# Performance work log

Measured on AMD Instinct MI355X. Metric: run time of the kernel, lower is better.

Reference implementation:

```python
import jax, jax.numpy as jnp
import numpy as np

N_NODES = 100000
N_EDGES = 1600000
IN_CH = 128
HID_CH = 128


def setup_inputs() -> dict:
    key = jax.random.key(0)
    ks = jax.random.split(key, 10)
    x = jax.random.normal(ks[0], (N_NODES, IN_CH), dtype=jnp.float32)
    edge_index = jax.random.randint(ks[1], (2, N_EDGES), 0, N_NODES, dtype=jnp.int64)
    s1 = 1.0 / np.sqrt(IN_CH)
    s2 = 1.0 / np.sqrt(HID_CH)
    return {
        "x": x,
        "edge_index": edge_index,
        "W1": jax.random.uniform(ks[2], (IN_CH, HID_CH), jnp.float32, -s1, s1),
        "b1": jnp.zeros((HID_CH,), jnp.float32),
        "W2": jax.random.uniform(ks[3], (HID_CH, HID_CH), jnp.float32, -s2, s2),
        "b2": jnp.zeros((HID_CH,), jnp.float32),
        "We": jax.random.uniform(ks[4], (IN_CH, HID_CH), jnp.float32, -s1, s1),
        "be": jax.random.uniform(ks[5], (HID_CH,), jnp.float32, -s1, s1),
        "Wfc": jax.random.uniform(ks[6], (HID_CH, 1), jnp.float32, -s2, s2),
        "bfc": jax.random.uniform(ks[7], (1,), jnp.float32, -s2, s2),
    }


def _gcn_conv(x, src, dst, norm, W, b, n_nodes):
    # PyG GCNConv: linear transform, then normalized scatter-add aggregation, then bias
    h = x @ W                                 # [N, H]
    msg = h[src] * norm[:, None]              # gather + scale  [E+N, H]
    out = jax.ops.segment_sum(msg, dst, num_segments=n_nodes)  # scatter-add [N, H]
    return out + b


def reference(x, edge_index, W1, b1, W2, b2, We, be, Wfc, bfc):
    n = x.shape[0]
    # add self-loops (PyG default add_self_loops=True)
    loop = jnp.arange(n, dtype=edge_index.dtype)
    src = jnp.concatenate([edge_index[0], loop])
    dst = jnp.concatenate([edge_index[1], loop])
    # symmetric degree normalization deg^-1/2 (edge_weight implicitly ones)
    deg = jax.ops.segment_sum(jnp.ones_like(src, dtype=x.dtype), dst, num_segments=n)
    dinv = jnp.where(deg > 0, jax.lax.rsqrt(deg), 0.0)
    norm = dinv[src] * dinv[dst]

    x_conv = jax.nn.relu(_gcn_conv(x, src, dst, norm, W1, b1, n))
    x_fc = jax.nn.relu(x @ We + be)
    h = x_conv + x_fc                          # residual; dropout is identity in eval
    x_conv2 = jax.nn.relu(_gcn_conv(h, src, dst, norm, W2, b2, n))
    h = x_conv2 + h
    # batch is all zeros -> global_mean_pool == mean over all nodes -> [1, H]
    pooled = jnp.mean(h, axis=0, keepdims=True)
    predict = jax.nn.sigmoid(pooled @ Wfc + bfc)  # [1, 1]
    return predict
```

## Files before the change

kernel.cpp:

```cpp
#include <hip/hip_runtime.h>
#include <hip/hip_bf16.h>

typedef unsigned int uint;
typedef unsigned short ushort;
typedef unsigned char uchar;
typedef __attribute__((ext_vector_type(8))) short short8;
typedef __attribute__((ext_vector_type(4))) float f32x4;

__device__ __forceinline__ float bf2f(ushort u) {
    union { uint i; float f; } v; v.i = ((uint)u) << 16; return v.f;
}
__device__ __forceinline__ ushort f2bf(float f) {
    union { float f; uint i; } v; v.f = f;
    uint x = v.i;
    uint r = (x + 0x7FFFu + ((x >> 16) & 1u)) >> 16;
    return (ushort)r;
}
__device__ __forceinline__ uchar f2q(float f) {
    return (uchar)(__builtin_amdgcn_cvt_pk_fp8_f32(f, 0.f, 0, false) & 0xFF);
}
__device__ __forceinline__ void q2f4(uint w, float* o) {
    o[0] = __builtin_amdgcn_cvt_f32_fp8(w, 0);
    o[1] = __builtin_amdgcn_cvt_f32_fp8(w, 1);
    o[2] = __builtin_amdgcn_cvt_f32_fp8(w, 2);
    o[3] = __builtin_amdgcn_cvt_f32_fp8(w, 3);
}


__global__ void k_degree(const int* __restrict__ dst, int* __restrict__ deg, int e) {
    int i = blockIdx.x * 256 + threadIdx.x;
    if (i < e) atomicAdd(&deg[dst[i]], 1);
}

__global__ void k_dinv(const int* __restrict__ deg, float* __restrict__ dinv, int n) {
    int i = blockIdx.x * 256 + threadIdx.x;
    if (i < n) dinv[i] = rsqrtf((float)deg[i] + 1.0f);
}

__global__ void k_scan_a(const int* __restrict__ deg, int* __restrict__ bsum, int n) {
    __shared__ int sd[256];
    int t = threadIdx.x;
    int base = blockIdx.x * 1024 + t * 4;
    int s = 0;
#pragma unroll
    for (int j = 0; j < 4; ++j) { int idx = base + j; if (idx < n) s += deg[idx]; }
    sd[t] = s; __syncthreads();
    for (int off = 1; off < 256; off <<= 1) {
        int v = (t >= off) ? sd[t - off] : 0;
        __syncthreads();
        sd[t] += v;
        __syncthreads();
    }
    if (t == 255) bsum[blockIdx.x] = sd[255];
}

__global__ void k_scan_b(const int* __restrict__ bsum, int* __restrict__ boff, int nb) {
    __shared__ int sd[256];
    int t = threadIdx.x;
    int v0 = (t < nb) ? bsum[t] : 0;
    sd[t] = v0; __syncthreads();
    for (int off = 1; off < 256; off <<= 1) {
        int v = (t >= off) ? sd[t - off] : 0;
        __syncthreads();
        sd[t] += v;
        __syncthreads();
    }
    if (t < nb) boff[t] = sd[t] - v0;
}

__global__ void k_scan_c(const int* __restrict__ deg, const int* __restrict__ boff,
                         int* __restrict__ offs, int n) {
    __shared__ int sd[256];
    int t = threadIdx.x;
    int base = blockIdx.x * 1024 + t * 4;
    int vals[4]; int s = 0;
#pragma unroll
    for (int j = 0; j < 4; ++j) {
        int idx = base + j;
        vals[j] = (idx < n) ? deg[idx] : 0;
        s += vals[j];
    }
    sd[t] = s; __syncthreads();
    for (int off = 1; off < 256; off <<= 1) {
        int v = (t >= off) ? sd[t - off] : 0;
        __syncthreads();
        sd[t] += v;
        __syncthreads();
    }
    int run = boff[blockIdx.x] + (sd[t] - s);
#pragma unroll
    for (int j = 0; j < 4; ++j) {
        int idx = base + j;
        if (idx < n) { offs[idx] = run; run += vals[j]; }
    }
}

__global__ void k_fill(const int* __restrict__ src, const int* __restrict__ dst,
                       const int* __restrict__ offs, int* __restrict__ cursor,
                       int* __restrict__ csr, int e) {
    int i = blockIdx.x * 256 + threadIdx.x;
    if (i < e) {
        int d = dst[i];
        int p = offs[d] + atomicAdd(&cursor[d], 1);
        csr[p] = src[i];
    }
}


__global__ __launch_bounds__(512) void k_gemm1(
    const float* __restrict__ x, const float* __restrict__ W1, const float* __restrict__ We,
    const float* __restrict__ be, const float* __restrict__ dinv,
    uchar* __restrict__ h1q, ushort* __restrict__ xfc, int n)
{
    __shared__ __align__(16) ushort Bt[256][72];
    int tid = threadIdx.x;
    int w = tid >> 6, lane = tid & 63;
    int ln15 = lane & 15, g = lane >> 4;
    int rowBase = blockIdx.x * 128 + w * 16;
    int r = rowBase + ln15;
    bool valid = r < n;

    short8 a[4];
#pragma unroll
    for (int ks = 0; ks < 4; ++ks) {
        float4 f0 = make_float4(0.f, 0.f, 0.f, 0.f), f1 = f0;
        if (valid) {
            const float* p = x + (size_t)r * 128 + ks * 32 + g * 8;
            f0 = *reinterpret_cast<const float4*>(p);
            f1 = *reinterpret_cast<const float4*>(p + 4);
        }
        short8 v;
        v[0] = (short)f2bf(f0.x); v[1] = (short)f2bf(f0.y);
        v[2] = (short)f2bf(f0.z); v[3] = (short)f2bf(f0.w);
        v[4] = (short)f2bf(f1.x); v[5] = (short)f2bf(f1.y);
        v[6] = (short)f2bf(f1.z); v[7] = (short)f2bf(f1.w);
        a[ks] = v;
    }

    f32x4 acc[16];
#pragma unroll
    for (int i = 0; i < 16; ++i) acc[i] = (f32x4){0.f, 0.f, 0.f, 0.f};

    for (int s = 0; s < 2; ++s) {
        for (int i = tid; i < 8192; i += 512) {
            int kl = i >> 7, j = i & 127;
            int kg = s * 64 + kl;
            Bt[j][kl]       = f2bf(W1[kg * 128 + j]);
            Bt[128 + j][kl] = f2bf(We[kg * 128 + j]);
        }
        __syncthreads();
#pragma unroll
        for (int t2 = 0; t2 < 2; ++t2) {
            short8 af = a[s * 2 + t2];
#pragma unroll
            for (int jf = 0; jf < 16; ++jf) {
                short8 bf = *reinterpret_cast<const short8*>(&Bt[jf * 16 + ln15][t2 * 32 + g * 8]);
                acc[jf] = __builtin_amdgcn_mfma_f32_16x16x32_bf16(af, bf, acc[jf], 0, 0, 0);
            }
        }
        __syncthreads();
    }

    float dv[4];
#pragma unroll
    for (int q = 0; q < 4; ++q) {
        int rr = rowBase + g * 4 + q;
        dv[q] = (rr < n) ? dinv[rr] : 0.f;
    }

#pragma unroll
    for (int jf = 0; jf < 16; ++jf) {
        int col = jf * 16 + ln15;
#pragma unroll
        for (int q = 0; q < 4; ++q) {
            int rr = rowBase + g * 4 + q;
            if (rr < n) {
                float v = acc[jf][q];
                if (col < 128) {
                    h1q[(size_t)rr * 128 + col] = f2q(v * dv[q]);
                } else {
                    float vv = fmaxf(v + be[col - 128], 0.f);
                    xfc[(size_t)rr * 128 + (col - 128)] = f2bf(vv);
                }
            }
        }
    }
}


__global__ __launch_bounds__(512) void k_gemm2(
    const ushort* __restrict__ h, const float* __restrict__ W2, const float* __restrict__ dinv,
    uchar* __restrict__ h2q, int n)
{
    __shared__ __align__(16) ushort Bt[128][72];
    int tid = threadIdx.x;
    int w = tid >> 6, lane = tid & 63;
    int ln15 = lane & 15, g = lane >> 4;
    int rowBase = blockIdx.x * 128 + w * 16;
    int r = rowBase + ln15;
    bool valid = r < n;

    short8 a[4];
#pragma unroll
    for (int ks = 0; ks < 4; ++ks) {
        short8 v = (short8){0,0,0,0,0,0,0,0};
        if (valid) v = *reinterpret_cast<const short8*>(h + (size_t)r * 128 + ks * 32 + g * 8);
        a[ks] = v;
    }

    f32x4 acc[8];
#pragma unroll
    for (int i = 0; i < 8; ++i) acc[i] = (f32x4){0.f, 0.f, 0.f, 0.f};

    for (int s = 0; s < 2; ++s) {
        for (int i = tid; i < 8192; i += 512) {
            int kl = i >> 7, j = i & 127;
            Bt[j][kl] = f2bf(W2[(s * 64 + kl) * 128 + j]);
        }
        __syncthreads();
#pragma unroll
        for (int t2 = 0; t2 < 2; ++t2) {
            short8 af = a[s * 2 + t2];
#pragma unroll
            for (int jf = 0; jf < 8; ++jf) {
                short8 bf = *reinterpret_cast<const short8*>(&Bt[jf * 16 + ln15][t2 * 32 + g * 8]);
                acc[jf] = __builtin_amdgcn_mfma_f32_16x16x32_bf16(af, bf, acc[jf], 0, 0, 0);
            }
        }
        __syncthreads();
    }

    float dv[4];
#pragma unroll
    for (int q = 0; q < 4; ++q) {
        int rr = rowBase + g * 4 + q;
        dv[q] = (rr < n) ? dinv[rr] : 0.f;
    }

#pragma unroll
    for (int jf = 0; jf < 8; ++jf) {
        int col = jf * 16 + ln15;
#pragma unroll
        for (int q = 0; q < 4; ++q) {
            int rr = rowBase + g * 4 + q;
            if (rr < n) h2q[(size_t)rr * 128 + col] = f2q(acc[jf][q] * dv[q]);
        }
    }
}


__global__ __launch_bounds__(256) void k_agg1(
    const int* __restrict__ csr, const int* __restrict__ offs, const int* __restrict__ degE,
    const float* __restrict__ dinv, const uchar* __restrict__ h1q, const ushort* __restrict__ xfc,
    const float* __restrict__ b1, ushort* __restrict__ h, int n)
{
    int t = threadIdx.x;
    int g = t >> 3, li = t & 7;
    int node = blockIdx.x * 32 + g;
    if (node >= n) return;
    int off = offs[node], cnt = degE[node];
    float di = dinv[node];
    int c0 = li * 16;
    float acc[16];
#pragma unroll
    for (int e = 0; e < 16; ++e) acc[e] = 0.f;

    for (int base = 0; base < cnt; base += 8) {
        int idx[8];
#pragma unroll
        for (int q = 0; q < 8; ++q) {
            int s = csr[off + base + q];
            idx[q] = (base + q < cnt) ? s : n;
        }
        uint4 u[8];
#pragma unroll
        for (int q = 0; q < 8; ++q)
            u[q] = *reinterpret_cast<const uint4*>(h1q + (size_t)idx[q] * 128 + c0);
#pragma unroll
        for (int q = 0; q < 8; ++q) {
            const uint* uw = reinterpret_cast<const uint*>(&u[q]);
#pragma unroll
            for (int p = 0; p < 4; ++p) {
                float d4[4]; q2f4(uw[p], d4);
                acc[4 * p + 0] += d4[0];
                acc[4 * p + 1] += d4[1];
                acc[4 * p + 2] += d4[2];
                acc[4 * p + 3] += d4[3];
            }
        }
    }

    uint4 us = *reinterpret_cast<const uint4*>(h1q + (size_t)node * 128 + c0);
    const uint* usw = reinterpret_cast<const uint*>(&us);
    float sdec[16];
#pragma unroll
    for (int p = 0; p < 4; ++p) q2f4(usw[p], &sdec[4 * p]);
    uint4 ux0 = *reinterpret_cast<const uint4*>(xfc + (size_t)node * 128 + c0);
    uint4 ux1 = *reinterpret_cast<const uint4*>(xfc + (size_t)node * 128 + c0 + 8);
    uint uxw[8] = {ux0.x, ux0.y, ux0.z, ux0.w, ux1.x, ux1.y, ux1.z, ux1.w};
    float bb[16];
#pragma unroll
    for (int p = 0; p < 4; ++p) {
        float4 bq = *reinterpret_cast<const float4*>(b1 + c0 + p * 4);
        bb[4 * p] = bq.x; bb[4 * p + 1] = bq.y; bb[4 * p + 2] = bq.z; bb[4 * p + 3] = bq.w;
    }
    uint outw[8];
#pragma unroll
    for (int j = 0; j < 8; ++j) {
        int e0 = 2 * j, e1 = 2 * j + 1;
        float v0 = fmaxf((acc[e0] + sdec[e0]) * di + bb[e0], 0.f) + bf2f((ushort)(uxw[j] & 0xffff));
        float v1 = fmaxf((acc[e1] + sdec[e1]) * di + bb[e1], 0.f) + bf2f((ushort)(uxw[j] >> 16));
        outw[j] = (uint)f2bf(v0) | ((uint)f2bf(v1) << 16);
    }
    ushort* hp = h + (size_t)node * 128 + c0;
    *reinterpret_cast<uint4*>(hp)     = make_uint4(outw[0], outw[1], outw[2], outw[3]);
    *reinterpret_cast<uint4*>(hp + 8) = make_uint4(outw[4], outw[5], outw[6], outw[7]);
}


__global__ __launch_bounds__(256) void k_agg2(
    const int* __restrict__ csr, const int* __restrict__ offs, const int* __restrict__ degE,
    const float* __restrict__ dinv, const uchar* __restrict__ h2q, const ushort* __restrict__ hres,
    const float* __restrict__ b2, float* __restrict__ pooled, int n)
{
    __shared__ float lpool[128];
    int t = threadIdx.x;
    if (t < 128) lpool[t] = 0.f;
    __syncthreads();
    int g = t >> 3, li = t & 7;
    int node = blockIdx.x * 32 + g;
    bool valid = node < n;
    int nodeC = valid ? node : (n - 1);
    int off = offs[nodeC];
    int cnt = valid ? degE[nodeC] : 0;
    float di = dinv[nodeC];
    int c0 = li * 16;
    float acc[16];
#pragma unroll
    for (int e = 0; e < 16; ++e) acc[e] = 0.f;

    for (int base = 0; base < cnt; base += 8) {
        int idx[8];
#pragma unroll
        for (int q = 0; q < 8; ++q) {
            int s = csr[off + base + q];
            idx[q] = (base + q < cnt) ? s : n;
        }
        uint4 u[8];
#pragma unroll
        for (int q = 0; q < 8; ++q)
            u[q] = *reinterpret_cast<const uint4*>(h2q + (size_t)idx[q] * 128 + c0);
#pragma unroll
        for (int q = 0; q < 8; ++q) {
            const uint* uw = reinterpret_cast<const uint*>(&u[q]);
#pragma unroll
            for (int p = 0; p < 4; ++p) {
                float d4[4]; q2f4(uw[p], d4);
                acc[4 * p + 0] += d4[0];
                acc[4 * p + 1] += d4[1];
                acc[4 * p + 2] += d4[2];
                acc[4 * p + 3] += d4[3];
            }
        }
    }

    uint4 us = *reinterpret_cast<const uint4*>(h2q + (size_t)nodeC * 128 + c0);
    const uint* usw = reinterpret_cast<const uint*>(&us);
    float sdec[16];
#pragma unroll
    for (int p = 0; p < 4; ++p) q2f4(usw[p], &sdec[4 * p]);
    uint4 ur0 = *reinterpret_cast<const uint4*>(hres + (size_t)nodeC * 128 + c0);
    uint4 ur1 = *reinterpret_cast<const uint4*>(hres + (size_t)nodeC * 128 + c0 + 8);
    uint urw[8] = {ur0.x, ur0.y, ur0.z, ur0.w, ur1.x, ur1.y, ur1.z, ur1.w};
    float bb[16];
#pragma unroll
    for (int p = 0; p < 4; ++p) {
        float4 bq = *reinterpret_cast<const float4*>(b2 + c0 + p * 4);
        bb[4 * p] = bq.x; bb[4 * p + 1] = bq.y; bb[4 * p + 2] = bq.z; bb[4 * p + 3] = bq.w;
    }
    float pv[16];
#pragma unroll
    for (int j = 0; j < 8; ++j) {
        int e0 = 2 * j, e1 = 2 * j + 1;
        pv[e0] = fmaxf((acc[e0] + sdec[e0]) * di + bb[e0], 0.f) + bf2f((ushort)(urw[j] & 0xffff));
        pv[e1] = fmaxf((acc[e1] + sdec[e1]) * di + bb[e1], 0.f) + bf2f((ushort)(urw[j] >> 16));
    }
    if (valid) {
#pragma unroll
        for (int e = 0; e < 16; ++e) atomicAdd(&lpool[c0 + e], pv[e]);
    }
    __syncthreads();
    if (t < 128) atomicAdd(&pooled[t], lpool[t]);
}


__global__ void k_final(const float* __restrict__ pooled, const float* __restrict__ Wfc,
                        const float* __restrict__ bfc, float* __restrict__ out, float invN) {
    int lane = threadIdx.x;
    float s = pooled[2 * lane] * invN * Wfc[2 * lane] +
              pooled[2 * lane + 1] * invN * Wfc[2 * lane + 1];
#pragma unroll
    for (int off = 32; off > 0; off >>= 1) s += __shfl_down(s, off);
    if (lane == 0) out[0] = 1.f / (1.f + expf(-(s + bfc[0])));
}


extern "C" void kernel_launch(void* const* d_in, const int* in_sizes, int n_in,
                              void* d_out, int out_size, void* d_ws, size_t ws_size,
                              hipStream_t stream) {
    const float* x   = (const float*)d_in[0];
    const int*   ei  = (const int*)d_in[1];
    const float* W1  = (const float*)d_in[2];
    const float* b1  = (const float*)d_in[3];
    const float* W2  = (const float*)d_in[4];
    const float* b2  = (const float*)d_in[5];
    const float* We  = (const float*)d_in[6];
    const float* be  = (const float*)d_in[7];
    const float* Wfc = (const float*)d_in[8];
    const float* bfc = (const float*)d_in[9];
    float* out = (float*)d_out;

    const int N = in_sizes[0] / 128;
    const int E = in_sizes[1] / 2;
    const int* src = ei;
    const int* dst = ei + E;

    char* w = (char*)d_ws;
    size_t off = 0;
    auto take = [&](size_t bytes) -> void* {
        void* p = w + off;
        off = (off + bytes + 255) & ~(size_t)255;
        return p;
    };
    int*    deg    = (int*)take((size_t)N * 4);
    int*    offs   = (int*)take((size_t)N * 4);
    int*    cursor = (int*)take((size_t)N * 4);
    float*  dinv   = (float*)take((size_t)N * 4);
    int*    bsum   = (int*)take(1024);
    int*    boff   = (int*)take(1024);
    int*    csr    = (int*)take((size_t)(E + 8) * 4);
    uchar*  h1q    = (uchar*)take((size_t)(N + 1) * 128);
    ushort* xfc    = (ushort*)take((size_t)N * 128 * 2);
    ushort* h      = (ushort*)take((size_t)N * 128 * 2);
    uchar*  h2q    = (uchar*)take((size_t)(N + 1) * 128);
    float*  pooled = (float*)take(512);

    const int nbE = (E + 255) / 256;
    const int nbScan = (N + 1023) / 1024;

    hipMemsetAsync(deg, 0, (size_t)N * 4, stream);
    hipMemsetAsync(cursor, 0, (size_t)N * 4, stream);
    hipMemsetAsync(pooled, 0, 512, stream);
    hipMemsetAsync(h1q + (size_t)N * 128, 0, 128, stream);
    hipMemsetAsync(h2q + (size_t)N * 128, 0, 128, stream);

    k_degree<<<nbE, 256, 0, stream>>>(dst, deg, E);
    k_dinv<<<(N + 255) / 256, 256, 0, stream>>>(deg, dinv, N);
    k_scan_a<<<nbScan, 256, 0, stream>>>(deg, bsum, N);
    k_scan_b<<<1, 256, 0, stream>>>(bsum, boff, nbScan);
    k_scan_c<<<nbScan, 256, 0, stream>>>(deg, boff, offs, N);
    k_fill<<<nbE, 256, 0, stream>>>(src, dst, offs, cursor, csr, E);

    k_gemm1<<<(N + 127) / 128, 512, 0, stream>>>(x, W1, We, be, dinv, h1q, xfc, N);
    k_agg1<<<(N + 31) / 32, 256, 0, stream>>>(csr, offs, deg, dinv, h1q, xfc, b1, h, N);
    k_gemm2<<<(N + 127) / 128, 512, 0, stream>>>(h, W2, dinv, h2q, N);
    k_agg2<<<(N + 31) / 32, 256, 0, stream>>>(csr, offs, deg, dinv, h2q, h, b2, pooled, N);
    k_final<<<1, 64, 0, stream>>>(pooled, Wfc, bfc, out, 1.0f / (float)N);
}
```

Measured before the change: 441.9 us.

## Bin degree/fill atomics by destination range and prefetch CSR indices in aggregation

```diff
diff --git a/kernel.cpp b/kernel.cpp
--- a/kernel.cpp
+++ b/kernel.cpp
@@ -27,9 +27,17 @@
 }
 
 
-__global__ void k_degree(const int* __restrict__ dst, int* __restrict__ deg, int e) {
-    int i = blockIdx.x * 256 + threadIdx.x;
-    if (i < e) atomicAdd(&deg[dst[i]], 1);
+__global__ void k_degree(const int* __restrict__ dst, int* __restrict__ deg,
+                         int e, int n) {
+    int bin = blockIdx.x & 7;
+    int sub = blockIdx.x >> 3;
+    int nsub = gridDim.x >> 3;
+    int q = (n + 7) >> 3;
+    int lo = bin * q, hi = min(n, lo + q);
+    for (int i = sub * 256 + threadIdx.x; i < e; i += nsub * 256) {
+        int d = dst[i];
+        if (d >= lo && d < hi) atomicAdd(&deg[d], 1);
+    }
 }
 
 __global__ void k_dinv(const int* __restrict__ deg, float* __restrict__ dinv, int n) {
@@ -97,12 +105,18 @@
 
 __global__ void k_fill(const int* __restrict__ src, const int* __restrict__ dst,
                        const int* __restrict__ offs, int* __restrict__ cursor,
-                       int* __restrict__ csr, int e) {
-    int i = blockIdx.x * 256 + threadIdx.x;
-    if (i < e) {
+                       int* __restrict__ csr, int e, int n) {
+    int bin = blockIdx.x & 7;
+    int sub = blockIdx.x >> 3;
+    int nsub = gridDim.x >> 3;
+    int q = (n + 7) >> 3;
+    int lo = bin * q, hi = min(n, lo + q);
+    for (int i = sub * 256 + threadIdx.x; i < e; i += nsub * 256) {
         int d = dst[i];
-        int p = offs[d] + atomicAdd(&cursor[d], 1);
-        csr[p] = src[i];
+        if (d >= lo && d < hi) {
+            int p = offs[d] + atomicAdd(&cursor[d], 1);
+            csr[p] = src[i];
+        }
     }
 }
 
@@ -265,17 +279,25 @@
 #pragma unroll
     for (int e = 0; e < 16; ++e) acc[e] = 0.f;
 
-    for (int base = 0; base < cnt; base += 8) {
-        int idx[8];
-#pragma unroll
-        for (int q = 0; q < 8; ++q) {
-            int s = csr[off + base + q];
-            idx[q] = (base + q < cnt) ? s : n;
-        }
+    int nbat = (cnt + 7) >> 3;
+    int idx[8];
+#pragma unroll
+    for (int q = 0; q < 8; ++q) {
+        int s = csr[off + q];
+        idx[q] = (q < cnt) ? s : n;
+    }
+    for (int b = 0; b < nbat; ++b) {
         uint4 u[8];
 #pragma unroll
         for (int q = 0; q < 8; ++q)
             u[q] = *reinterpret_cast<const uint4*>(h1q + (size_t)idx[q] * 128 + c0);
+        int base2 = (b + 1) * 8;
+        int idxn[8];
+#pragma unroll
+        for (int q = 0; q < 8; ++q) {
+            int s = csr[off + base2 + q];
+            idxn[q] = (base2 + q < cnt) ? s : n;
+        }
 #pragma unroll
         for (int q = 0; q < 8; ++q) {
             const uint* uw = reinterpret_cast<const uint*>(&u[q]);
@@ -288,6 +310,8 @@
                 acc[4 * p + 3] += d4[3];
             }
         }
+#pragma unroll
+        for (int q = 0; q < 8; ++q) idx[q] = idxn[q];
     }
 
     uint4 us = *reinterpret_cast<const uint4*>(h1q + (size_t)node * 128 + c0);
@@ -339,17 +363,25 @@
 #pragma unroll
     for (int e = 0; e < 16; ++e) acc[e] = 0.f;
 
-    for (int base = 0; base < cnt; base += 8) {
-        int idx[8];
-#pragma unroll
-        for (int q = 0; q < 8; ++q) {
-            int s = csr[off + base + q];
-            idx[q] = (base + q < cnt) ? s : n;
-        }
+    int nbat = (cnt + 7) >> 3;
+    int idx[8];
+#pragma unroll
+    for (int q = 0; q < 8; ++q) {
+        int s = csr[off + q];
+        idx[q] = (q < cnt) ? s : n;
+    }
+    for (int b = 0; b < nbat; ++b) {
         uint4 u[8];
 #pragma unroll
         for (int q = 0; q < 8; ++q)
             u[q] = *reinterpret_cast<const uint4*>(h2q + (size_t)idx[q] * 128 + c0);
+        int base2 = (b + 1) * 8;
+        int idxn[8];
+#pragma unroll
+        for (int q = 0; q < 8; ++q) {
+            int s = csr[off + base2 + q];
+            idxn[q] = (base2 + q < cnt) ? s : n;
+        }
 #pragma unroll
         for (int q = 0; q < 8; ++q) {
             const uint* uw = reinterpret_cast<const uint*>(&u[q]);
@@ -362,6 +394,8 @@
                 acc[4 * p + 3] += d4[3];
             }
         }
+#pragma unroll
+        for (int q = 0; q < 8; ++q) idx[q] = idxn[q];
     }
 
     uint4 us = *reinterpret_cast<const uint4*>(h2q + (size_t)nodeC * 128 + c0);
@@ -438,14 +472,13 @@
     float*  dinv   = (float*)take((size_t)N * 4);
     int*    bsum   = (int*)take(1024);
     int*    boff   = (int*)take(1024);
-    int*    csr    = (int*)take((size_t)(E + 8) * 4);
+    int*    csr    = (int*)take((size_t)(E + 64) * 4);
     uchar*  h1q    = (uchar*)take((size_t)(N + 1) * 128);
     ushort* xfc    = (ushort*)take((size_t)N * 128 * 2);
     ushort* h      = (ushort*)take((size_t)N * 128 * 2);
     uchar*  h2q    = (uchar*)take((size_t)(N + 1) * 128);
     float*  pooled = (float*)take(512);
 
-    const int nbE = (E + 255) / 256;
     const int nbScan = (N + 1023) / 1024;
 
     hipMemsetAsync(deg, 0, (size_t)N * 4, stream);
@@ -454,12 +487,12 @@
     hipMemsetAsync(h1q + (size_t)N * 128, 0, 128, stream);
     hipMemsetAsync(h2q + (size_t)N * 128, 0, 128, stream);
 
-    k_degree<<<nbE, 256, 0, stream>>>(dst, deg, E);
+    k_degree<<<2048, 256, 0, stream>>>(dst, deg, E, N);
     k_dinv<<<(N + 255) / 256, 256, 0, stream>>>(deg, dinv, N);
     k_scan_a<<<nbScan, 256, 0, stream>>>(deg, bsum, N);
     k_scan_b<<<1, 256, 0, stream>>>(bsum, boff, nbScan);
     k_scan_c<<<nbScan, 256, 0, stream>>>(deg, boff, offs, N);
-    k_fill<<<nbE, 256, 0, stream>>>(src, dst, offs, cursor, csr, E);
+    k_fill<<<2048, 256, 0, stream>>>(src, dst, offs, cursor, csr, E, N);
 
     k_gemm1<<<(N + 127) / 128, 512, 0, stream>>>(x, W1, We, be, dinv, h1q, xfc, N);
     k_agg1<<<(N + 31) / 32, 256, 0, stream>>>(csr, offs, deg, dinv, h1q, xfc, b1, h, N);
```

New measurement: 422.7 us. -4.3%, faster.
